# Optimization experiments

Measured on AMD Instinct MI355X. Metric: run time of the kernel, lower is better.

The kernel has to match this reference:

```python
import jax, jax.numpy as jnp
import numpy as np

IMAGE_SIZE = 1024      # config.model.image_size
DOWNSIZING = 64        # PromptGetter grid cell size (in upsampled pixels)
THRESHOLD = 0.65       # default_threshold_target
NUM_BG = 1             # num_bg_points
EPS = 1e-12


def setup_inputs() -> dict:
    key = jax.random.key(0)
    k1, k2 = jax.random.split(key)
    image_embeddings = jax.random.normal(k1, (1, 256, 64, 64), dtype=jnp.float32)
    reference_feats = jax.random.normal(k2, (32, 1, 256), dtype=jnp.float32)
    return {"image_embeddings": image_embeddings, "reference_feats": reference_feats}


def _point_selection(sim_up):
    """sim_up: [S, S] similarity map at original resolution.
    Returns (points_scores [n_cells, 3] as (x, y, score) sorted by score desc,
             bg_coords [NUM_BG, 2] as (x, y)).
    Faithful static-shape version of PromptGetter._point_selection: the torch
    code picks, within every DOWNSIZING x DOWNSIZING grid cell, the highest-sim
    pixel above threshold; cells with no pixel above threshold yield -1 rows."""
    n = IMAGE_SIZE // DOWNSIZING  # 16 -> 256 grid cells
    # background point: global minimum of the similarity map
    flat = sim_up.reshape(-1)
    _, bg_idx = jax.lax.top_k(-flat, NUM_BG)
    bg_row = bg_idx // IMAGE_SIZE
    bg_col = bg_idx % IMAGE_SIZE
    bg_coords = jnp.stack([bg_col, bg_row], axis=-1).astype(jnp.float32)  # (x, y)

    # foreground: per-grid-cell argmax
    cells = sim_up.reshape(n, DOWNSIZING, n, DOWNSIZING)
    cells = cells.transpose(0, 2, 1, 3).reshape(n * n, DOWNSIZING * DOWNSIZING)
    local_idx = jnp.argmax(cells, axis=-1)                                   # [n*n]
    score = jnp.take_along_axis(cells, local_idx[:, None], axis=-1)[:, 0]    # [n*n]
    cell_ids = jnp.arange(n * n)
    cy, cx = cell_ids // n, cell_ids % n
    ly, lx = local_idx // DOWNSIZING, local_idx % DOWNSIZING
    y = (cy * DOWNSIZING + ly).astype(jnp.float32)
    x = (cx * DOWNSIZING + lx).astype(jnp.float32)
    pts = jnp.stack([x, y, score], axis=-1)                                   # [n*n, 3]
    valid = score > THRESHOLD
    pts = jnp.where(valid[:, None], pts, jnp.float32(-1.0))
    order = jnp.argsort(-pts[:, 2])  # sort by score, descending; -1 rows sink
    return pts[order], bg_coords


def reference(image_embeddings, reference_feats):
    # image_embeddings: [1, C, h, w]; reference_feats: [L, 1, C]
    feat = image_embeddings[0]                                   # [C, h, w]
    C, h, w = feat.shape
    feat = feat / (jnp.linalg.norm(feat, axis=0, keepdims=True) + EPS)
    feat = feat.reshape(C, h * w)                                # [C, h*w]
    ref = reference_feats[:, 0, :]                               # [L, C]
    ref = ref / (jnp.linalg.norm(ref, axis=-1, keepdims=True) + EPS)
    sim = (ref @ feat).reshape(-1, h, w)                         # [L, h, w] cosine sim
    # postprocess_masks with original_size == image_size: one bilinear upsample
    sim_up = jax.image.resize(sim, (sim.shape[0], IMAGE_SIZE, IMAGE_SIZE), method="bilinear")
    total_points_scores, total_bg_coords = jax.vmap(_point_selection)(sim_up)
    return total_points_scores, total_bg_coords
```

## Files before the change

kernel.cpp:

```cpp
#include <hip/hip_runtime.h>
#include <math.h>

#define THRESH 0.65f

__device__ float g_sim[32 * 4096];

__global__ __launch_bounds__(256) void k_sim(const float* __restrict__ feat,
                                             const float* __restrict__ ref) {
    __shared__ float rn0[256], rn1[256], red[256];
    __shared__ float pd0[256], pd1[256], pn[256];
    int t = threadIdx.x;
    int m0 = blockIdx.y * 2;

    float v0 = ref[m0 * 256 + t];
    float v1 = ref[(m0 + 1) * 256 + t];
    red[t] = v0 * v0;
    __syncthreads();
    for (int s = 128; s > 0; s >>= 1) { if (t < s) red[t] += red[t + s]; __syncthreads(); }
    float den0 = sqrtf(red[0]) + 1e-12f;
    __syncthreads();
    red[t] = v1 * v1;
    __syncthreads();
    for (int s = 128; s > 0; s >>= 1) { if (t < s) red[t] += red[t + s]; __syncthreads(); }
    float den1 = sqrtf(red[0]) + 1e-12f;
    rn0[t] = v0 / den0;
    rn1[t] = v1 / den1;
    __syncthreads();

    int half = t >> 7, pxl = t & 127;
    int px = blockIdx.x * 128 + pxl;
    const float* fp = feat + px + half * 128 * 4096;
    const float* r0 = rn0 + half * 128;
    const float* r1 = rn1 + half * 128;
    float d0 = 0.f, d1 = 0.f, nq = 0.f;
    for (int g = 0; g < 8; ++g) {
#pragma unroll
        for (int cc = 0; cc < 16; ++cc) {
            int c = g * 16 + cc;
            float fv = fp[c * 4096];
            d0 += fv * r0[c];
            d1 += fv * r1[c];
            nq += fv * fv;
        }
    }
    pd0[t] = d0; pd1[t] = d1; pn[t] = nq;
    __syncthreads();
    float D0 = pd0[pxl] + pd0[pxl + 128];
    float D1 = pd1[pxl] + pd1[pxl + 128];
    float NQ = pn[pxl] + pn[pxl + 128];
    float den = sqrtf(NQ) + 1e-12f;
    g_sim[(m0 + half) * 4096 + px] = (half ? D1 : D0) / den;
}

__global__ __launch_bounds__(256) void k_scan_out(float* __restrict__ out) {
    __shared__ float S[64 * 65];
    __shared__ float sc[256];
    __shared__ float wmin[4];
    __shared__ int wmini[4];

    int m = blockIdx.x, t = threadIdx.x;
    const float* sm = g_sim + m * 4096;
    for (int k = 0; k < 16; ++k) {
        int f = t + 256 * k;
        S[(f >> 6) * 65 + (f & 63)] = sm[f];
    }
    __syncthreads();

    int cy = t >> 4, cx = t & 15;
    int gxs[6];
#pragma unroll
    for (int j = 0; j < 6; ++j) {
        int g = 4 * cx - 1 + j;
        gxs[j] = min(max(g, 0), 63);
    }
    const int   L0[5]  = {0, 8, 24, 40, 56};
    const int   L1[5]  = {7, 23, 39, 55, 63};
    const float WXA[5] = {0.53125f, 0.03125f, 0.03125f, 0.03125f, 0.03125f};
    const float WXB[5] = {0.96875f, 0.96875f, 0.96875f, 0.96875f, 0.46875f};
    const float WCA[5] = {0.46875f, 0.96875f, 0.96875f, 0.96875f, 0.96875f};
    const float WCB[5] = {0.03125f, 0.03125f, 0.03125f, 0.03125f, 0.53125f};

    float bmax = -1e30f, bmin = 1e30f;
    int bmaxi = 0, bmini = 0;
#pragma unroll
    for (int sy = 0; sy < 5; ++sy) {
#pragma unroll
        for (int e = 0; e < 2; ++e) {
            int r = e ? L1[sy] : L0[sy];
            int oy = cy * 64 + r;
            float fy = (oy + 0.5f) * 0.0625f - 0.5f;
            float y0f = floorf(fy);
            float wy = fy - y0f, w1y = 1.0f - wy;
            bool ylo = fy < 0.0f, yhi = fy > 63.0f;
            int y0 = (int)y0f;
            const float* P0 = S + min(max(y0, 0), 63) * 65;
            const float* P1 = S + min(max(y0 + 1, 0), 63) * 65;
            float q[6];
#pragma unroll
            for (int j = 0; j < 6; ++j) {
                float a = P0[gxs[j]], c = P1[gxs[j]];
                q[j] = ylo ? a : (yhi ? c : w1y * a + wy * c);
            }
#pragma unroll
            for (int s5 = 0; s5 < 5; ++s5) {
                float q0 = q[s5], q1 = q[s5 + 1];
                float va, vb;
                if (cx == 0 && s5 == 0)       { va = q1; vb = q1; }
                else if (cx == 15 && s5 == 4) { va = q0; vb = q0; }
                else {
                    va = WCA[s5] * q0 + WXA[s5] * q1;
                    vb = WCB[s5] * q0 + WXB[s5] * q1;
                }
                float smax, smin; int smaxl, sminl;
                if (va >= vb) { smax = va; smaxl = L0[s5]; } else { smax = vb; smaxl = L1[s5]; }
                if (va <= vb) { smin = va; sminl = L0[s5]; } else { smin = vb; sminl = L1[s5]; }
                if (smax > bmax) { bmax = smax; bmaxi = r * 64 + smaxl; }
                if (smin < bmin) { bmin = smin; bmini = oy * 1024 + cx * 64 + sminl; }
            }
        }
    }

    bool valid = bmax > THRESH;
    float px = valid ? (float)(cx * 64 + (bmaxi & 63)) : -1.0f;
    float py = valid ? (float)(cy * 64 + (bmaxi >> 6)) : -1.0f;
    float ps = valid ? bmax : -1.0f;
    sc[t] = ps;
    __syncthreads();
    int rank = 0;
    for (int j = 0; j < 256; ++j) {
        float sj = sc[j];
        rank += (sj > ps || (sj == ps && j < t)) ? 1 : 0;
    }
    float* o = out + m * 768 + rank * 3;
    o[0] = px; o[1] = py; o[2] = ps;

    for (int off = 32; off > 0; off >>= 1) {
        float mv = __shfl_down(bmin, off);
        int   mj = __shfl_down(bmini, off);
        if (mv < bmin || (mv == bmin && mj < bmini)) { bmin = mv; bmini = mj; }
    }
    if ((t & 63) == 0) { wmin[t >> 6] = bmin; wmini[t >> 6] = bmini; }
    __syncthreads();
    if (t == 0) {
        float bv = wmin[0]; int bi = wmini[0];
        for (int w = 1; w < 4; ++w) {
            if (wmin[w] < bv || (wmin[w] == bv && wmini[w] < bi)) {
                bv = wmin[w]; bi = wmini[w];
            }
        }
        out[24576 + m * 2 + 0] = (float)(bi % 1024);
        out[24576 + m * 2 + 1] = (float)(bi / 1024);
    }
}

extern "C" void kernel_launch(void* const* d_in, const int* in_sizes, int n_in,
                              void* d_out, int out_size, void* d_ws, size_t ws_size,
                              hipStream_t stream) {
    const float* feat = (const float*)d_in[0];
    const float* ref  = (const float*)d_in[1];
    if (in_sizes[0] == 32 * 256) {
        feat = (const float*)d_in[1];
        ref  = (const float*)d_in[0];
    }
    float* out = (float*)d_out;
    (void)d_ws; (void)ws_size;

    k_sim<<<dim3(32, 16), 256, 0, stream>>>(feat, ref);
    k_scan_out<<<32, 256, 0, stream>>>(out);
}
```

Measured before the change: 74.76 us.

## Fuse similarity and point-selection kernels via last-block atomic counter

```diff
diff --git a/kernel.cpp b/kernel.cpp
--- a/kernel.cpp
+++ b/kernel.cpp
@@ -4,11 +4,19 @@
 #define THRESH 0.65f
 
 __device__ float g_sim[32 * 4096];
+__device__ int g_cnt[16];
 
-__global__ __launch_bounds__(256) void k_sim(const float* __restrict__ feat,
-                                             const float* __restrict__ ref) {
+__global__ __launch_bounds__(256) void k_fused(const float* __restrict__ feat,
+                                               const float* __restrict__ ref,
+                                               float* __restrict__ out) {
     __shared__ float rn0[256], rn1[256], red[256];
     __shared__ float pd0[256], pd1[256], pn[256];
+    __shared__ float S[64 * 65];
+    __shared__ float sc[256];
+    __shared__ float wmin[4];
+    __shared__ int wmini[4];
+    __shared__ int s_last;
+
     int t = threadIdx.x;
     int m0 = blockIdx.y * 2;
 
@@ -50,21 +58,17 @@
     float NQ = pn[pxl] + pn[pxl + 128];
     float den = sqrtf(NQ) + 1e-12f;
     g_sim[(m0 + half) * 4096 + px] = (half ? D1 : D0) / den;
-}
 
-__global__ __launch_bounds__(256) void k_scan_out(float* __restrict__ out) {
-    __shared__ float S[64 * 65];
-    __shared__ float sc[256];
-    __shared__ float wmin[4];
-    __shared__ int wmini[4];
-
-    int m = blockIdx.x, t = threadIdx.x;
-    const float* sm = g_sim + m * 4096;
-    for (int k = 0; k < 16; ++k) {
-        int f = t + 256 * k;
-        S[(f >> 6) * 65 + (f & 63)] = sm[f];
+    __threadfence();
+    __syncthreads();
+    if (t == 0) {
+        int old = atomicAdd(&g_cnt[blockIdx.y], 1);
+        s_last = (old == 31);
     }
     __syncthreads();
+    if (!s_last) return;
+    __threadfence();
+    if (t == 0) g_cnt[blockIdx.y] = 0;
 
     int cy = t >> 4, cx = t & 15;
     int gxs[6];
@@ -80,76 +84,87 @@
     const float WCA[5] = {0.46875f, 0.96875f, 0.96875f, 0.96875f, 0.96875f};
     const float WCB[5] = {0.03125f, 0.03125f, 0.03125f, 0.03125f, 0.53125f};
 
-    float bmax = -1e30f, bmin = 1e30f;
-    int bmaxi = 0, bmini = 0;
+    for (int mm = 0; mm < 2; ++mm) {
+        int m = m0 + mm;
+        const float* sm = g_sim + m * 4096;
+        __syncthreads();
+        for (int k = 0; k < 16; ++k) {
+            int f = t + 256 * k;
+            S[(f >> 6) * 65 + (f & 63)] = sm[f];
+        }
+        __syncthreads();
+
+        float bmax = -1e30f, bmin = 1e30f;
+        int bmaxi = 0, bmini = 0;
 #pragma unroll
-    for (int sy = 0; sy < 5; ++sy) {
+        for (int sy = 0; sy < 5; ++sy) {
 #pragma unroll
-        for (int e = 0; e < 2; ++e) {
-            int r = e ? L1[sy] : L0[sy];
-            int oy = cy * 64 + r;
-            float fy = (oy + 0.5f) * 0.0625f - 0.5f;
-            float y0f = floorf(fy);
-            float wy = fy - y0f, w1y = 1.0f - wy;
-            bool ylo = fy < 0.0f, yhi = fy > 63.0f;
-            int y0 = (int)y0f;
-            const float* P0 = S + min(max(y0, 0), 63) * 65;
-            const float* P1 = S + min(max(y0 + 1, 0), 63) * 65;
-            float q[6];
+            for (int e = 0; e < 2; ++e) {
+                int r = e ? L1[sy] : L0[sy];
+                int oy = cy * 64 + r;
+                float fy = (oy + 0.5f) * 0.0625f - 0.5f;
+                float y0f = floorf(fy);
+                float wy = fy - y0f, w1y = 1.0f - wy;
+                bool ylo = fy < 0.0f, yhi = fy > 63.0f;
+                int y0 = (int)y0f;
+                const float* P0 = S + min(max(y0, 0), 63) * 65;
+                const float* P1 = S + min(max(y0 + 1, 0), 63) * 65;
+                float q[6];
 #pragma unroll
-            for (int j = 0; j < 6; ++j) {
-                float a = P0[gxs[j]], c = P1[gxs[j]];
-                q[j] = ylo ? a : (yhi ? c : w1y * a + wy * c);
-            }
+                for (int j = 0; j < 6; ++j) {
+                    float a = P0[gxs[j]], c = P1[gxs[j]];
+                    q[j] = ylo ? a : (yhi ? c : w1y * a + wy * c);
+                }
 #pragma unroll
-            for (int s5 = 0; s5 < 5; ++s5) {
-                float q0 = q[s5], q1 = q[s5 + 1];
-                float va, vb;
-                if (cx == 0 && s5 == 0)       { va = q1; vb = q1; }
-                else if (cx == 15 && s5 == 4) { va = q0; vb = q0; }
-                else {
-                    va = WCA[s5] * q0 + WXA[s5] * q1;
-                    vb = WCB[s5] * q0 + WXB[s5] * q1;
+                for (int s5 = 0; s5 < 5; ++s5) {
+                    float q0 = q[s5], q1 = q[s5 + 1];
+                    float va, vb;
+                    if (cx == 0 && s5 == 0)       { va = q1; vb = q1; }
+                    else if (cx == 15 && s5 == 4) { va = q0; vb = q0; }
+                    else {
+                        va = WCA[s5] * q0 + WXA[s5] * q1;
+                        vb = WCB[s5] * q0 + WXB[s5] * q1;
+                    }
+                    float smax, smin; int smaxl, sminl;
+                    if (va >= vb) { smax = va; smaxl = L0[s5]; } else { smax = vb; smaxl = L1[s5]; }
+                    if (va <= vb) { smin = va; sminl = L0[s5]; } else { smin = vb; sminl = L1[s5]; }
+                    if (smax > bmax) { bmax = smax; bmaxi = r * 64 + smaxl; }
+                    if (smin < bmin) { bmin = smin; bmini = oy * 1024 + cx * 64 + sminl; }
                 }
-                float smax, smin; int smaxl, sminl;
-                if (va >= vb) { smax = va; smaxl = L0[s5]; } else { smax = vb; smaxl = L1[s5]; }
-                if (va <= vb) { smin = va; sminl = L0[s5]; } else { smin = vb; sminl = L1[s5]; }
-                if (smax > bmax) { bmax = smax; bmaxi = r * 64 + smaxl; }
-                if (smin < bmin) { bmin = smin; bmini = oy * 1024 + cx * 64 + sminl; }
             }
         }
-    }
 
-    bool valid = bmax > THRESH;
-    float px = valid ? (float)(cx * 64 + (bmaxi & 63)) : -1.0f;
-    float py = valid ? (float)(cy * 64 + (bmaxi >> 6)) : -1.0f;
-    float ps = valid ? bmax : -1.0f;
-    sc[t] = ps;
-    __syncthreads();
-    int rank = 0;
-    for (int j = 0; j < 256; ++j) {
-        float sj = sc[j];
-        rank += (sj > ps || (sj == ps && j < t)) ? 1 : 0;
-    }
-    float* o = out + m * 768 + rank * 3;
-    o[0] = px; o[1] = py; o[2] = ps;
+        bool valid = bmax > THRESH;
+        float opx = valid ? (float)(cx * 64 + (bmaxi & 63)) : -1.0f;
+        float opy = valid ? (float)(cy * 64 + (bmaxi >> 6)) : -1.0f;
+        float ops = valid ? bmax : -1.0f;
+        sc[t] = ops;
+        __syncthreads();
+        int rank = 0;
+        for (int j = 0; j < 256; ++j) {
+            float sj = sc[j];
+            rank += (sj > ops || (sj == ops && j < t)) ? 1 : 0;
+        }
+        float* o = out + m * 768 + rank * 3;
+        o[0] = opx; o[1] = opy; o[2] = ops;
 
-    for (int off = 32; off > 0; off >>= 1) {
-        float mv = __shfl_down(bmin, off);
-        int   mj = __shfl_down(bmini, off);
-        if (mv < bmin || (mv == bmin && mj < bmini)) { bmin = mv; bmini = mj; }
-    }
-    if ((t & 63) == 0) { wmin[t >> 6] = bmin; wmini[t >> 6] = bmini; }
-    __syncthreads();
-    if (t == 0) {
-        float bv = wmin[0]; int bi = wmini[0];
-        for (int w = 1; w < 4; ++w) {
-            if (wmin[w] < bv || (wmin[w] == bv && wmini[w] < bi)) {
-                bv = wmin[w]; bi = wmini[w];
+        for (int off = 32; off > 0; off >>= 1) {
+            float mv = __shfl_down(bmin, off);
+            int   mj = __shfl_down(bmini, off);
+            if (mv < bmin || (mv == bmin && mj < bmini)) { bmin = mv; bmini = mj; }
+        }
+        if ((t & 63) == 0) { wmin[t >> 6] = bmin; wmini[t >> 6] = bmini; }
+        __syncthreads();
+        if (t == 0) {
+            float bv = wmin[0]; int bi = wmini[0];
+            for (int w = 1; w < 4; ++w) {
+                if (wmin[w] < bv || (wmin[w] == bv && wmini[w] < bi)) {
+                    bv = wmin[w]; bi = wmini[w];
+                }
             }
+            out[24576 + m * 2 + 0] = (float)(bi % 1024);
+            out[24576 + m * 2 + 1] = (float)(bi / 1024);
         }
-        out[24576 + m * 2 + 0] = (float)(bi % 1024);
-        out[24576 + m * 2 + 1] = (float)(bi / 1024);
     }
 }
 
@@ -165,6 +180,5 @@
     float* out = (float*)d_out;
     (void)d_ws; (void)ws_size;
 
-    k_sim<<<dim3(32, 16), 256, 0, stream>>>(feat, ref);
-    k_scan_out<<<32, 256, 0, stream>>>(out);
+    k_fused<<<dim3(32, 16), 256, 0, stream>>>(feat, ref, out);
 }
```

After: 142.0 us. +90.0%, slower.
